# Kernel optimization log

Measured on AMD Instinct MI355X. Metric: run time of the kernel, lower is better.

The kernel has to match this reference:

```python
import jax, jax.numpy as jnp
import numpy as np

EMBED_DIM = 128
NUM_HEADS = 4
WH, WW = 7, 7
N = WH * WW
HEAD_DIM = EMBED_DIM // NUM_HEADS
SCALE = HEAD_DIM ** -0.5


def _rel_position_index():
    # double_step_seq(2*Ww-1, Wh, 1, Ww), then idx = coords + coords.T, flip cols
    seq1 = np.arange(0, (2 * WW - 1) * WH, 2 * WW - 1)
    seq2 = np.arange(0, WW)
    coords = (seq1[:, None] + seq2[None, :]).reshape(1, -1)  # (1, N)
    idx = coords + coords.T                                   # (N, N)
    idx = idx[:, ::-1].copy()                                 # flip(1)
    return jnp.asarray(idx, dtype=jnp.int32)

REL_IDX = _rel_position_index()


def setup_inputs() -> dict:
    key = jax.random.key(0)
    ks = jax.random.split(key, 8)
    B = 4096
    nW = 64
    C = EMBED_DIM
    x = jax.random.normal(ks[0], (B, N, C), dtype=jnp.float32)
    # shift mask: values in (-inf, 0]; emulate with -100 on ~half the entries
    mask = jnp.where(jax.random.uniform(ks[1], (nW, N, N)) > 0.5, -100.0, 0.0).astype(jnp.float32)
    lim = 1.0 / np.sqrt(C)
    qkv_w = jax.random.uniform(ks[2], (3 * C, C), minval=-lim, maxval=lim, dtype=jnp.float32)
    qkv_b = jax.random.uniform(ks[3], (3 * C,), minval=-lim, maxval=lim, dtype=jnp.float32)
    proj_w = jax.random.uniform(ks[4], (C, C), minval=-lim, maxval=lim, dtype=jnp.float32)
    proj_b = jax.random.uniform(ks[5], (C,), minval=-lim, maxval=lim, dtype=jnp.float32)
    n_rel = (2 * WH - 1) * (2 * WW - 1)
    bias_table = 0.02 * jax.random.normal(ks[6], (n_rel, NUM_HEADS), dtype=jnp.float32)
    return {"x": x, "mask": mask, "qkv_w": qkv_w, "qkv_b": qkv_b,
            "proj_w": proj_w, "proj_b": proj_b, "bias_table": bias_table}


def reference(x, mask, qkv_w, qkv_b, proj_w, proj_b, bias_table):
    B, n, C = x.shape
    H, D = NUM_HEADS, HEAD_DIM
    qkv = x @ qkv_w.T + qkv_b                       # (B, N, 3C)
    qkv = qkv.reshape(B, n, 3, H, D).transpose(2, 0, 3, 1, 4)
    q, k, v = qkv[0], qkv[1], qkv[2]                # each (B, H, N, D)
    attn = jnp.einsum('bhnd,bhmd->bhnm', q * SCALE, k)
    # relative position bias gather: (N, N, H) -> (H, N, N)
    rel_bias = bias_table[REL_IDX.reshape(-1)].reshape(n, n, H).transpose(2, 0, 1)
    attn = attn + rel_bias[None]
    nW = mask.shape[0]
    attn = attn.reshape(B // nW, nW, H, n, n) + mask[None, :, None]
    attn = attn.reshape(B, H, n, n)
    attn = jax.nn.softmax(attn, axis=-1)
    out = jnp.einsum('bhnm,bhmd->bhnd', attn, v)    # (B, H, N, D)
    out = out.transpose(0, 2, 1, 3).reshape(B, n, C)
    return out @ proj_w.T + proj_b
```

## Files before the change

### kernel.cpp

```cpp
#include <hip/hip_runtime.h>


typedef __bf16 bf16_t;
typedef __bf16 bf8v  __attribute__((ext_vector_type(8)));
typedef __bf16 bf4v  __attribute__((ext_vector_type(4)));
typedef float  f4v   __attribute__((ext_vector_type(4)));

#define QK_SCALE 0.17677669529663687f

__device__ __forceinline__ f4v mfma16(bf8v a, bf8v b, f4v c) {
  return __builtin_amdgcn_mfma_f32_16x16x32_bf16(a, b, c, 0, 0, 0);
}

__device__ __forceinline__ bf8v join8(bf4v lo, bf4v hi) {
  return __builtin_shufflevector(lo, hi, 0, 1, 2, 3, 4, 5, 6, 7);
}

__global__ void prep_kernel(const float* __restrict__ mask,
                            const float* __restrict__ qkv_w,
                            const float* __restrict__ proj_w,
                            const float* __restrict__ bias_table,
                            bf16_t* __restrict__ wq,
                            bf16_t* __restrict__ wp,
                            float* __restrict__ cbs) {
  const int stride = gridDim.x * blockDim.x;
  const int tid0 = blockIdx.x * blockDim.x + threadIdx.x;
  for (int i = tid0; i < 24 * 4 * 64 * 8; i += stride) {
    int j = i & 7, l = (i >> 3) & 63, kt = (i >> 9) & 3, t = i >> 11;
    int n = t * 16 + (l & 15), k = kt * 32 + (l >> 4) * 8 + j;
    wq[i] = (bf16_t)qkv_w[n * 128 + k];
  }
  for (int i = tid0; i < 8 * 4 * 64 * 8; i += stride) {
    int j = i & 7, l = (i >> 3) & 63, kt = (i >> 9) & 3, t = i >> 11;
    int n = t * 16 + (l & 15), k = kt * 32 + (l >> 4) * 8 + j;
    wp[i] = (bf16_t)proj_w[n * 128 + k];
  }
  for (int i = tid0; i < 64 * 4 * 64 * 64; i += stride) {
    int j = i & 63;
    int l16 = j >> 2, nt = j & 3;
    int m = nt * 16 + l16;
    int n = (i >> 6) & 63, h = (i >> 12) & 3, w = i >> 14;
    float v;
    if (m >= 49) {
      v = 0.0f;
    } else if (n >= 49) {
      v = 1.0f;
    } else {
      int cn = 13 * (n / 7) + n % 7;
      int mm = 48 - m;
      int cm = 13 * (mm / 7) + mm % 7;
      v = __expf(bias_table[(cn + cm) * 4 + h] + mask[(w * 49 + n) * 49 + m]);
    }
    cbs[i] = v;
  }
}

__global__ __launch_bounds__(256, 4) void msa_kernel(
    const float* __restrict__ x,
    const float* __restrict__ qkv_b,
    const float* __restrict__ proj_b,
    const bf16_t* __restrict__ wq,
    const bf16_t* __restrict__ wp,
    const float* __restrict__ cbs,
    float* __restrict__ out) {
  __shared__ __align__(16) bf16_t gA[8704];
  __shared__ __align__(16) bf16_t gT[4][2560];

#define AS(r, c)    gA[(r) * 136 + (c)]
#define VTT(hh, d, t) gA[((hh) * 32 + (d)) * 68 + (t)]
#define TT(hh, r, c)  gT[hh][(r) * 40 + (c)]

  const int tid = threadIdx.x;
  const int wv  = tid >> 6;
  const int ln  = tid & 63;
  const int l16 = ln & 15;
  const int l4  = ln >> 4;
  const int b   = blockIdx.x;
  const int w   = b & 63;
  const int h   = wv;

  {
    const float4* xb = (const float4*)(x + (size_t)b * (49 * 128));
    for (int i = tid; i < 64 * 32; i += 256) {
      int r = i >> 5, c4 = (i & 31) << 2;
      float4 v;
      if (r < 49) v = xb[(r * 128 + c4) >> 2];
      else        v = make_float4(0.f, 0.f, 0.f, 0.f);
      bf4v o = { (bf16_t)v.x, (bf16_t)v.y, (bf16_t)v.z, (bf16_t)v.w };
      *(bf4v*)&AS(r, c4) = o;
    }
  }
  __syncthreads();

  f4v acc[4][4];
#pragma unroll
  for (int ti = 0; ti < 4; ++ti)
#pragma unroll
    for (int mt = 0; mt < 4; ++mt) acc[ti][mt] = (f4v){0.f, 0.f, 0.f, 0.f};
#pragma unroll
  for (int kt = 0; kt < 4; ++kt) {
    bf8v a[4];
#pragma unroll
    for (int mt = 0; mt < 4; ++mt)
      a[mt] = *(const bf8v*)&AS(mt * 16 + l16, kt * 32 + l4 * 8);
    bf8v bb[4];
#pragma unroll
    for (int ti = 0; ti < 4; ++ti) {
      int t = (ti < 2) ? (2 * h + ti) : (8 + 2 * h + (ti - 2));
      bb[ti] = *(const bf8v*)(wq + (((t * 4 + kt) * 64 + ln) << 3));
    }
#pragma unroll
    for (int ti = 0; ti < 4; ++ti)
#pragma unroll
      for (int mt = 0; mt < 4; ++mt)
        acc[ti][mt] = mfma16(a[mt], bb[ti], acc[ti][mt]);
  }

  bf8v kf[4], qf[4];
#pragma unroll
  for (int ti = 0; ti < 2; ++ti) {
    float bias = qkv_b[128 + 32 * h + ti * 16 + l16];
#pragma unroll
    for (int mt = 0; mt < 4; ++mt)
#pragma unroll
      for (int r = 0; r < 4; ++r)
        TT(h, mt * 16 + l4 * 4 + r, ti * 16 + l16) = (bf16_t)(acc[2 + ti][mt][r] + bias);
  }
#pragma unroll
  for (int mt = 0; mt < 4; ++mt)
    kf[mt] = *(const bf8v*)&TT(h, mt * 16 + l16, l4 * 8);

#pragma unroll
  for (int ti = 0; ti < 2; ++ti) {
    float bias = qkv_b[32 * h + ti * 16 + l16];
#pragma unroll
    for (int mt = 0; mt < 4; ++mt)
#pragma unroll
      for (int r = 0; r < 4; ++r)
        TT(h, mt * 16 + l4 * 4 + r, ti * 16 + l16) =
            (bf16_t)((acc[ti][mt][r] + bias) * QK_SCALE);
  }
#pragma unroll
  for (int mt = 0; mt < 4; ++mt)
    qf[mt] = *(const bf8v*)&TT(h, mt * 16 + l16, l4 * 8);

  f4v lg[4][4];
#pragma unroll
  for (int mt = 0; mt < 4; ++mt)
#pragma unroll
    for (int nt = 0; nt < 4; ++nt)
      lg[mt][nt] = mfma16(qf[mt], kf[nt], (f4v){0.f, 0.f, 0.f, 0.f});

  const float* cbp = cbs + ((size_t)(w * 4 + h) << 12);
  float ph1[4][4][2];
#pragma unroll
  for (int mt = 0; mt < 4; ++mt) {
#pragma unroll
    for (int r = 0; r < 4; ++r) {
      int row = mt * 16 + l4 * 4 + r;
      float4 e = *(const float4*)(cbp + (row << 6) + l16 * 4);
      float p0 = __expf(lg[mt][0][r]) * e.x;
      float p1 = __expf(lg[mt][1][r]) * e.y;
      float p2 = __expf(lg[mt][2][r]) * e.z;
      float p3 = __expf(lg[mt][3][r]) * e.w;
      TT(h, row, l16)      = (bf16_t)p0;
      TT(h, row, 16 + l16) = (bf16_t)p1;
      ph1[mt][r][0] = p2;
      ph1[mt][r][1] = p3;
    }
  }

  f4v vacc[2][4];
#pragma unroll
  for (int ti = 0; ti < 2; ++ti)
#pragma unroll
    for (int mt = 0; mt < 4; ++mt) vacc[ti][mt] = (f4v){0.f, 0.f, 0.f, 0.f};
#pragma unroll
  for (int kt = 0; kt < 4; ++kt) {
    bf8v a[4];
#pragma unroll
    for (int mt = 0; mt < 4; ++mt)
      a[mt] = *(const bf8v*)&AS(mt * 16 + l16, kt * 32 + l4 * 8);
    bf8v bb[2];
#pragma unroll
    for (int ti = 0; ti < 2; ++ti) {
      int t = 16 + 2 * h + ti;
      bb[ti] = *(const bf8v*)(wq + (((t * 4 + kt) * 64 + ln) << 3));
    }
#pragma unroll
    for (int ti = 0; ti < 2; ++ti)
#pragma unroll
      for (int mt = 0; mt < 4; ++mt)
        vacc[ti][mt] = mfma16(a[mt], bb[ti], vacc[ti][mt]);
  }

  __syncthreads();

#pragma unroll
  for (int ti = 0; ti < 2; ++ti) {
    float bias = qkv_b[256 + 32 * h + ti * 16 + l16];
#pragma unroll
    for (int mt = 0; mt < 4; ++mt) {
      bf4v o = { (bf16_t)(vacc[ti][mt][0] + bias), (bf16_t)(vacc[ti][mt][1] + bias),
                 (bf16_t)(vacc[ti][mt][2] + bias), (bf16_t)(vacc[ti][mt][3] + bias) };
      *(bf4v*)&VTT(h, ti * 16 + l16, mt * 16 + l4 * 4) = o;
    }
  }

  const bf16_t one16 = (bf16_t)1.0f;
  const bf8v ones = { one16, one16, one16, one16, one16, one16, one16, one16 };
  f4v oc[4][2], sacc[4];
#pragma unroll
  for (int nt = 0; nt < 4; ++nt) {
    sacc[nt] = (f4v){0.f, 0.f, 0.f, 0.f};
#pragma unroll
    for (int dt = 0; dt < 2; ++dt) oc[nt][dt] = (f4v){0.f, 0.f, 0.f, 0.f};
  }
  {
    bf8v pf[4], vf[2];
#pragma unroll
    for (int nt = 0; nt < 4; ++nt) pf[nt] = *(const bf8v*)&TT(h, nt * 16 + l16, l4 * 8);
#pragma unroll
    for (int dt = 0; dt < 2; ++dt)
      vf[dt] = join8(*(const bf4v*)&VTT(h, dt * 16 + l16, l4 * 8),
                     *(const bf4v*)&VTT(h, dt * 16 + l16, l4 * 8 + 4));
#pragma unroll
    for (int nt = 0; nt < 4; ++nt) {
#pragma unroll
      for (int dt = 0; dt < 2; ++dt) oc[nt][dt] = mfma16(pf[nt], vf[dt], oc[nt][dt]);
      sacc[nt] = mfma16(pf[nt], ones, sacc[nt]);
    }
#pragma unroll
    for (int mt = 0; mt < 4; ++mt)
#pragma unroll
      for (int r = 0; r < 4; ++r) {
        int row = mt * 16 + l4 * 4 + r;
        TT(h, row, l16)      = (bf16_t)ph1[mt][r][0];
        TT(h, row, 16 + l16) = (bf16_t)ph1[mt][r][1];
      }
#pragma unroll
    for (int nt = 0; nt < 4; ++nt) pf[nt] = *(const bf8v*)&TT(h, nt * 16 + l16, l4 * 8);
#pragma unroll
    for (int dt = 0; dt < 2; ++dt)
      vf[dt] = join8(*(const bf4v*)&VTT(h, dt * 16 + l16, 32 + l4 * 8),
                     *(const bf4v*)&VTT(h, dt * 16 + l16, 32 + l4 * 8 + 4));
#pragma unroll
    for (int nt = 0; nt < 4; ++nt) {
#pragma unroll
      for (int dt = 0; dt < 2; ++dt) oc[nt][dt] = mfma16(pf[nt], vf[dt], oc[nt][dt]);
      sacc[nt] = mfma16(pf[nt], ones, sacc[nt]);
    }
  }

#pragma unroll
  for (int nt = 0; nt < 4; ++nt) {
    float inv[4];
#pragma unroll
    for (int r = 0; r < 4; ++r) inv[r] = 1.0f / sacc[nt][r];
#pragma unroll
    for (int dt = 0; dt < 2; ++dt)
#pragma unroll
      for (int r = 0; r < 4; ++r)
        TT(h, nt * 16 + l4 * 4 + r, dt * 16 + l16) = (bf16_t)(oc[nt][dt][r] * inv[r]);
  }

  __syncthreads();

  {
    f4v pacc[4][2];
#pragma unroll
    for (int mt = 0; mt < 4; ++mt)
#pragma unroll
      for (int nj = 0; nj < 2; ++nj) pacc[mt][nj] = (f4v){0.f, 0.f, 0.f, 0.f};
#pragma unroll
    for (int kt = 0; kt < 4; ++kt) {
      bf8v a[4];
#pragma unroll
      for (int mt = 0; mt < 4; ++mt)
        a[mt] = *(const bf8v*)&TT(kt, mt * 16 + l16, l4 * 8);
      bf8v bwv[2];
#pragma unroll
      for (int nj = 0; nj < 2; ++nj) {
        int t = wv * 2 + nj;
        bwv[nj] = *(const bf8v*)(wp + (((t * 4 + kt) * 64 + ln) << 3));
      }
#pragma unroll
      for (int mt = 0; mt < 4; ++mt)
#pragma unroll
        for (int nj = 0; nj < 2; ++nj)
          pacc[mt][nj] = mfma16(a[mt], bwv[nj], pacc[mt][nj]);
    }
    float* ob = out + (size_t)b * (49 * 128);
#pragma unroll
    for (int nj = 0; nj < 2; ++nj) {
      int c = (wv * 2 + nj) * 16 + l16;
      float pb = proj_b[c];
#pragma unroll
      for (int mt = 0; mt < 4; ++mt) {
#pragma unroll
        for (int r = 0; r < 4; ++r) {
          int row = mt * 16 + l4 * 4 + r;
          if (row < 49) ob[row * 128 + c] = pacc[mt][nj][r] + pb;
        }
      }
    }
  }
}

extern "C" void kernel_launch(void* const* d_in, const int* in_sizes, int n_in,
                              void* d_out, int out_size, void* d_ws, size_t ws_size,
                              hipStream_t stream) {
  const float* x          = (const float*)d_in[0];
  const float* mask       = (const float*)d_in[1];
  const float* qkv_w      = (const float*)d_in[2];
  const float* qkv_b      = (const float*)d_in[3];
  const float* proj_w     = (const float*)d_in[4];
  const float* proj_b     = (const float*)d_in[5];
  const float* bias_table = (const float*)d_in[6];

  char* ws = (char*)d_ws;
  bf16_t* wq = (bf16_t*)ws;
  bf16_t* wp = (bf16_t*)(ws + 98304);
  float*  cbs = (float*)(ws + 131072);

  prep_kernel<<<1024, 256, 0, stream>>>(mask, qkv_w, proj_w, bias_table, wq, wp, cbs);
  msa_kernel<<<4096, 256, 0, stream>>>(x, qkv_b, proj_b, wq, wp, cbs, (float*)d_out);
}
```

Measured before the change: 282.7 us.

## Transpose MFMA operand order so accumulators write vectorized bf16 rows to LDS

Swaps the A/B operands of the QKV, QK^T, PV and row-sum MFMAs so each lane holds four consecutive columns of one row. This lets results go to shared memory as packed 4-wide bf16 stores instead of scalar scattered stores. The precomputed exp(bias+mask) table is re-laid out to match the new accumulator layout, so each lane reads it with a contiguous float4. The V transpose pitch is padded to 72 so one aligned 8-wide load replaces two 4-wide loads. The aim is fewer LDS instructions and bank conflicts, at the cost of a bit more shared memory per block and reliance on the swapped-layout indexing being exactly right.

```diff
diff --git a/kernel.cpp b/kernel.cpp
--- a/kernel.cpp
+++ b/kernel.cpp
@@ -10,10 +10,6 @@
 
 __device__ __forceinline__ f4v mfma16(bf8v a, bf8v b, f4v c) {
   return __builtin_amdgcn_mfma_f32_16x16x32_bf16(a, b, c, 0, 0, 0);
-}
-
-__device__ __forceinline__ bf8v join8(bf4v lo, bf4v hi) {
-  return __builtin_shufflevector(lo, hi, 0, 1, 2, 3, 4, 5, 6, 7);
 }
 
 __global__ void prep_kernel(const float* __restrict__ mask,
@@ -35,11 +31,15 @@
     int n = t * 16 + (l & 15), k = kt * 32 + (l >> 4) * 8 + j;
     wp[i] = (bf16_t)proj_w[n * 128 + k];
   }
-  for (int i = tid0; i < 64 * 4 * 64 * 64; i += stride) {
-    int j = i & 63;
-    int l16 = j >> 2, nt = j & 3;
-    int m = nt * 16 + l16;
-    int n = (i >> 6) & 63, h = (i >> 12) & 3, w = i >> 14;
+  for (int i = tid0; i < 64 * 4 * 4 * 4 * 64 * 4; i += stride) {
+    int r  = i & 3;
+    int ln = (i >> 2) & 63;
+    int mt = (i >> 8) & 3;
+    int nt = (i >> 10) & 3;
+    int h  = (i >> 12) & 3;
+    int w  = i >> 14;
+    int n = nt * 16 + (ln & 15);
+    int m = mt * 16 + (ln >> 4) * 4 + r;
     float v;
     if (m >= 49) {
       v = 0.0f;
@@ -63,11 +63,11 @@
     const bf16_t* __restrict__ wp,
     const float* __restrict__ cbs,
     float* __restrict__ out) {
-  __shared__ __align__(16) bf16_t gA[8704];
+  __shared__ __align__(16) bf16_t gA[9216];
   __shared__ __align__(16) bf16_t gT[4][2560];
 
-#define AS(r, c)    gA[(r) * 136 + (c)]
-#define VTT(hh, d, t) gA[((hh) * 32 + (d)) * 68 + (t)]
+#define AS(r, c)      gA[(r) * 136 + (c)]
+#define VTT(hh, d, t) gA[((hh) * 32 + (d)) * 72 + (t)]
 #define TT(hh, r, c)  gT[hh][(r) * 40 + (c)]
 
   const int tid = threadIdx.x;
@@ -113,18 +113,20 @@
     for (int ti = 0; ti < 4; ++ti)
 #pragma unroll
       for (int mt = 0; mt < 4; ++mt)
-        acc[ti][mt] = mfma16(a[mt], bb[ti], acc[ti][mt]);
+        acc[ti][mt] = mfma16(bb[ti], a[mt], acc[ti][mt]);
   }
 
   bf8v kf[4], qf[4];
 #pragma unroll
   for (int ti = 0; ti < 2; ++ti) {
-    float bias = qkv_b[128 + 32 * h + ti * 16 + l16];
-#pragma unroll
-    for (int mt = 0; mt < 4; ++mt)
-#pragma unroll
-      for (int r = 0; r < 4; ++r)
-        TT(h, mt * 16 + l4 * 4 + r, ti * 16 + l16) = (bf16_t)(acc[2 + ti][mt][r] + bias);
+    float4 kb = *(const float4*)(qkv_b + 128 + 32 * h + 16 * ti + 4 * l4);
+#pragma unroll
+    for (int mt = 0; mt < 4; ++mt) {
+      f4v v = acc[2 + ti][mt];
+      bf4v o = { (bf16_t)(v[0] + kb.x), (bf16_t)(v[1] + kb.y),
+                 (bf16_t)(v[2] + kb.z), (bf16_t)(v[3] + kb.w) };
+      *(bf4v*)&TT(h, mt * 16 + l16, ti * 16 + 4 * l4) = o;
+    }
   }
 #pragma unroll
   for (int mt = 0; mt < 4; ++mt)
@@ -132,13 +134,14 @@
 
 #pragma unroll
   for (int ti = 0; ti < 2; ++ti) {
-    float bias = qkv_b[32 * h + ti * 16 + l16];
-#pragma unroll
-    for (int mt = 0; mt < 4; ++mt)
-#pragma unroll
-      for (int r = 0; r < 4; ++r)
-        TT(h, mt * 16 + l4 * 4 + r, ti * 16 + l16) =
-            (bf16_t)((acc[ti][mt][r] + bias) * QK_SCALE);
+    float4 qb = *(const float4*)(qkv_b + 32 * h + 16 * ti + 4 * l4);
+#pragma unroll
+    for (int mt = 0; mt < 4; ++mt) {
+      f4v v = acc[ti][mt];
+      bf4v o = { (bf16_t)((v[0] + qb.x) * QK_SCALE), (bf16_t)((v[1] + qb.y) * QK_SCALE),
+                 (bf16_t)((v[2] + qb.z) * QK_SCALE), (bf16_t)((v[3] + qb.w) * QK_SCALE) };
+      *(bf4v*)&TT(h, mt * 16 + l16, ti * 16 + 4 * l4) = o;
+    }
   }
 #pragma unroll
   for (int mt = 0; mt < 4; ++mt)
@@ -146,29 +149,31 @@
 
   f4v lg[4][4];
 #pragma unroll
-  for (int mt = 0; mt < 4; ++mt)
+  for (int mtk = 0; mtk < 4; ++mtk)
 #pragma unroll
     for (int nt = 0; nt < 4; ++nt)
-      lg[mt][nt] = mfma16(qf[mt], kf[nt], (f4v){0.f, 0.f, 0.f, 0.f});
+      lg[mtk][nt] = mfma16(kf[mtk], qf[nt], (f4v){0.f, 0.f, 0.f, 0.f});
 
   const float* cbp = cbs + ((size_t)(w * 4 + h) << 12);
-  float ph1[4][4][2];
-#pragma unroll
-  for (int mt = 0; mt < 4; ++mt) {
-#pragma unroll
-    for (int r = 0; r < 4; ++r) {
-      int row = mt * 16 + l4 * 4 + r;
-      float4 e = *(const float4*)(cbp + (row << 6) + l16 * 4);
-      float p0 = __expf(lg[mt][0][r]) * e.x;
-      float p1 = __expf(lg[mt][1][r]) * e.y;
-      float p2 = __expf(lg[mt][2][r]) * e.z;
-      float p3 = __expf(lg[mt][3][r]) * e.w;
-      TT(h, row, l16)      = (bf16_t)p0;
-      TT(h, row, 16 + l16) = (bf16_t)p1;
-      ph1[mt][r][0] = p2;
-      ph1[mt][r][1] = p3;
-    }
-  }
+#pragma unroll
+  for (int nt = 0; nt < 4; ++nt) {
+#pragma unroll
+    for (int mtk = 0; mtk < 4; ++mtk) {
+      float4 e = *(const float4*)(cbp + ((((nt * 4 + mtk) << 6) | ln) << 2));
+      lg[mtk][nt][0] = __expf(lg[mtk][nt][0]) * e.x;
+      lg[mtk][nt][1] = __expf(lg[mtk][nt][1]) * e.y;
+      lg[mtk][nt][2] = __expf(lg[mtk][nt][2]) * e.z;
+      lg[mtk][nt][3] = __expf(lg[mtk][nt][3]) * e.w;
+    }
+  }
+#pragma unroll
+  for (int nt = 0; nt < 4; ++nt)
+#pragma unroll
+    for (int mtk = 0; mtk < 2; ++mtk) {
+      f4v p = lg[mtk][nt];
+      bf4v o = { (bf16_t)p[0], (bf16_t)p[1], (bf16_t)p[2], (bf16_t)p[3] };
+      *(bf4v*)&TT(h, nt * 16 + l16, mtk * 16 + 4 * l4) = o;
+    }
 
   f4v vacc[2][4];
 #pragma unroll
@@ -209,59 +214,55 @@
 
   const bf16_t one16 = (bf16_t)1.0f;
   const bf8v ones = { one16, one16, one16, one16, one16, one16, one16, one16 };
-  f4v oc[4][2], sacc[4];
+  f4v oc[2][4], sacc[4];
 #pragma unroll
   for (int nt = 0; nt < 4; ++nt) {
     sacc[nt] = (f4v){0.f, 0.f, 0.f, 0.f};
 #pragma unroll
-    for (int dt = 0; dt < 2; ++dt) oc[nt][dt] = (f4v){0.f, 0.f, 0.f, 0.f};
+    for (int dt = 0; dt < 2; ++dt) oc[dt][nt] = (f4v){0.f, 0.f, 0.f, 0.f};
   }
   {
     bf8v pf[4], vf[2];
 #pragma unroll
     for (int nt = 0; nt < 4; ++nt) pf[nt] = *(const bf8v*)&TT(h, nt * 16 + l16, l4 * 8);
 #pragma unroll
+    for (int dt = 0; dt < 2; ++dt) vf[dt] = *(const bf8v*)&VTT(h, dt * 16 + l16, l4 * 8);
+#pragma unroll
     for (int dt = 0; dt < 2; ++dt)
-      vf[dt] = join8(*(const bf4v*)&VTT(h, dt * 16 + l16, l4 * 8),
-                     *(const bf4v*)&VTT(h, dt * 16 + l16, l4 * 8 + 4));
-#pragma unroll
-    for (int nt = 0; nt < 4; ++nt) {
-#pragma unroll
-      for (int dt = 0; dt < 2; ++dt) oc[nt][dt] = mfma16(pf[nt], vf[dt], oc[nt][dt]);
-      sacc[nt] = mfma16(pf[nt], ones, sacc[nt]);
-    }
-#pragma unroll
-    for (int mt = 0; mt < 4; ++mt)
-#pragma unroll
-      for (int r = 0; r < 4; ++r) {
-        int row = mt * 16 + l4 * 4 + r;
-        TT(h, row, l16)      = (bf16_t)ph1[mt][r][0];
-        TT(h, row, 16 + l16) = (bf16_t)ph1[mt][r][1];
+#pragma unroll
+      for (int nt = 0; nt < 4; ++nt) oc[dt][nt] = mfma16(vf[dt], pf[nt], oc[dt][nt]);
+#pragma unroll
+    for (int nt = 0; nt < 4; ++nt) sacc[nt] = mfma16(ones, pf[nt], sacc[nt]);
+#pragma unroll
+    for (int nt = 0; nt < 4; ++nt)
+#pragma unroll
+      for (int mtk = 2; mtk < 4; ++mtk) {
+        f4v p = lg[mtk][nt];
+        bf4v o = { (bf16_t)p[0], (bf16_t)p[1], (bf16_t)p[2], (bf16_t)p[3] };
+        *(bf4v*)&TT(h, nt * 16 + l16, (mtk - 2) * 16 + 4 * l4) = o;
       }
 #pragma unroll
     for (int nt = 0; nt < 4; ++nt) pf[nt] = *(const bf8v*)&TT(h, nt * 16 + l16, l4 * 8);
 #pragma unroll
+    for (int dt = 0; dt < 2; ++dt) vf[dt] = *(const bf8v*)&VTT(h, dt * 16 + l16, 32 + l4 * 8);
+#pragma unroll
     for (int dt = 0; dt < 2; ++dt)
-      vf[dt] = join8(*(const bf4v*)&VTT(h, dt * 16 + l16, 32 + l4 * 8),
-                     *(const bf4v*)&VTT(h, dt * 16 + l16, 32 + l4 * 8 + 4));
-#pragma unroll
-    for (int nt = 0; nt < 4; ++nt) {
-#pragma unroll
-      for (int dt = 0; dt < 2; ++dt) oc[nt][dt] = mfma16(pf[nt], vf[dt], oc[nt][dt]);
-      sacc[nt] = mfma16(pf[nt], ones, sacc[nt]);
-    }
+#pragma unroll
+      for (int nt = 0; nt < 4; ++nt) oc[dt][nt] = mfma16(vf[dt], pf[nt], oc[dt][nt]);
+#pragma unroll
+    for (int nt = 0; nt < 4; ++nt) sacc[nt] = mfma16(ones, pf[nt], sacc[nt]);
   }
 
 #pragma unroll
   for (int nt = 0; nt < 4; ++nt) {
-    float inv[4];
-#pragma unroll
-    for (int r = 0; r < 4; ++r) inv[r] = 1.0f / sacc[nt][r];
-#pragma unroll
-    for (int dt = 0; dt < 2; ++dt)
-#pragma unroll
-      for (int r = 0; r < 4; ++r)
-        TT(h, nt * 16 + l4 * 4 + r, dt * 16 + l16) = (bf16_t)(oc[nt][dt][r] * inv[r]);
+    float inv = 1.0f / sacc[nt][0];
+#pragma unroll
+    for (int dt = 0; dt < 2; ++dt) {
+      f4v v = oc[dt][nt];
+      bf4v o = { (bf16_t)(v[0] * inv), (bf16_t)(v[1] * inv),
+                 (bf16_t)(v[2] * inv), (bf16_t)(v[3] * inv) };
+      *(bf4v*)&TT(h, nt * 16 + l16, dt * 16 + 4 * l4) = o;
+    }
   }
 
   __syncthreads();
```

Result: faster. 264.6 us (-6.4%).
